# Kernel tuning notes

Hardware: AMD Instinct MI355X
Metric: run time of the kernel (lower is better)

Reference implementation:

```python
import jax, jax.numpy as jnp
import numpy as np

D_MODEL = 768
NUM_HEADS = 12
D_K = D_MODEL // NUM_HEADS
B, S = 2, 4096


def setup_inputs() -> dict:
    key = jax.random.key(0)
    ks = jax.random.split(key, 11)
    lim = 1.0 / np.sqrt(D_MODEL)  # torch Linear default init range
    def lin(k1, k2):
        W = jax.random.uniform(k1, (D_MODEL, D_MODEL), jnp.float32, -lim, lim)
        b = jax.random.uniform(k2, (D_MODEL,), jnp.float32, -lim, lim)
        return W, b
    Wq, bq = lin(ks[0], ks[1])
    Wk, bk = lin(ks[2], ks[3])
    Wv, bv = lin(ks[4], ks[5])
    Wo, bo = lin(ks[6], ks[7])
    Q = jax.random.normal(ks[8], (B, S, D_MODEL), jnp.float32)
    K = jax.random.normal(ks[9], (B, S, D_MODEL), jnp.float32)
    V = jax.random.normal(ks[10], (B, S, D_MODEL), jnp.float32)
    return {"Q": Q, "K": K, "V": V,
            "Wq": Wq, "bq": bq, "Wk": Wk, "bk": bk,
            "Wv": Wv, "bv": bv, "Wo": Wo, "bo": bo}


def reference(Q, K, V, Wq, bq, Wk, bk, Wv, bv, Wo, bo):
    def split_heads(x):
        b, s, _ = x.shape
        return x.reshape(b, s, NUM_HEADS, D_K).transpose(0, 2, 1, 3)  # [B,H,S,d_k]

    q = split_heads(Q @ Wq.T + bq)
    k = split_heads(K @ Wk.T + bk)
    v = split_heads(V @ Wv.T + bv)

    scale = 1.0 / np.sqrt(D_K).astype(np.float32)
    scores = jnp.einsum('bhqd,bhkd->bhqk', q, k) * scale  # [B,H,S,S]
    probs = jax.nn.softmax(scores, axis=-1)
    attn = jnp.einsum('bhqk,bhkd->bhqd', probs, v)  # [B,H,S,d_k]

    out = attn.transpose(0, 2, 1, 3).reshape(Q.shape[0], Q.shape[1], D_MODEL)
    return out @ Wo.T + bo
```

## Files before the change

### kernel.cpp

```cpp
#include <hip/hip_runtime.h>
#include <hip/hip_bf16.h>
#include <stdint.h>

#define DM 768
#define DK 64
#define NH 12
#define SQ 4096
#define BB 2

typedef __attribute__((ext_vector_type(8))) short bf16x8;
typedef __attribute__((ext_vector_type(4))) float f32x4;
typedef __attribute__((ext_vector_type(16))) float f32x16;
typedef __attribute__((ext_vector_type(4))) unsigned short u16x4;
typedef __attribute__((ext_vector_type(4))) unsigned int u32x4;
typedef unsigned short u16;
typedef unsigned int   u32;

__device__ __forceinline__ u16 f2bf(float f) {
    u32 u = __builtin_bit_cast(u32, f);
    u32 r = (u + 0x7fffu + ((u >> 16) & 1u)) >> 16;
    return (u16)r;
}
__device__ __forceinline__ u32 pack_trunc(float lo, float hi) {
    return __builtin_amdgcn_perm(__builtin_bit_cast(u32, hi),
                                 __builtin_bit_cast(u32, lo), 0x07060302u);
}
__device__ __forceinline__ void gl_lds16(const u16* g, u16* l) {
    __builtin_amdgcn_global_load_lds(
        (const __attribute__((address_space(1))) void*)g,
        (__attribute__((address_space(3))) void*)l, 16, 0, 0);
}

__global__ __launch_bounds__(256) void cvt_w(
    const float* __restrict__ W0, const float* __restrict__ W1,
    const float* __restrict__ W2, const float* __restrict__ W3,
    u16* __restrict__ d0, u16* __restrict__ d1,
    u16* __restrict__ d2, u16* __restrict__ d3)
{
    const float* s = blockIdx.y == 0 ? W0 : blockIdx.y == 1 ? W1
                   : blockIdx.y == 2 ? W2 : W3;
    u16* d        = blockIdx.y == 0 ? d0 : blockIdx.y == 1 ? d1
                   : blockIdx.y == 2 ? d2 : d3;
    size_t i = ((size_t)blockIdx.x * 256 + threadIdx.x) * 8;
    float4 a = *(const float4*)&s[i];
    float4 b = *(const float4*)&s[i + 4];
    u16x4 lo, hi;
    lo.x = f2bf(a.x); lo.y = f2bf(a.y); lo.z = f2bf(a.z); lo.w = f2bf(a.w);
    hi.x = f2bf(b.x); hi.y = f2bf(b.y); hi.z = f2bf(b.z); hi.w = f2bf(b.w);
    *(u16x4*)&d[i]     = lo;
    *(u16x4*)&d[i + 4] = hi;
}

#define BM 128
#define BN 128

__global__ __launch_bounds__(256) void gemm_qkv(
    const float* __restrict__ A0, const float* __restrict__ A1,
    const float* __restrict__ A2,
    const u16* __restrict__ W0, const u16* __restrict__ W1,
    const u16* __restrict__ W2,
    const float* __restrict__ b0, const float* __restrict__ b1,
    const float* __restrict__ b2,
    u16* __restrict__ qo, u16* __restrict__ ko, u16* __restrict__ vto,
    float qscale)
{
    __shared__ __align__(16) u16 Asm[2][BM * 32];
    __shared__ __align__(16) u16 Bsm[2][BM * 32];

    const int tid  = threadIdx.x;
    const int lane = tid & 63;
    const int w    = tid >> 6;
    const int wr   = w >> 1, wc = w & 1;
    const int l16  = lane & 15, lg = lane >> 4;

    const int ntiles = DM / BN;
    const int mt = blockIdx.x / ntiles;
    const int nt = blockIdx.x % ntiles;
    const int m0 = mt * BM, n0 = nt * BN;

    const int op = blockIdx.y;
    const float* A    = op == 0 ? A0 : op == 1 ? A1 : A2;
    const u16*  W     = op == 0 ? W0 : op == 1 ? W1 : W2;
    const float* bias = op == 0 ? b0 : op == 1 ? b1 : b2;
    const float oscale = op == 0 ? qscale : 1.0f;

    f32x4 acc[4][4];
    #pragma unroll
    for (int mi = 0; mi < 4; ++mi)
        #pragma unroll
        for (int ni = 0; ni < 4; ++ni)
            #pragma unroll
            for (int r = 0; r < 4; ++r) acc[mi][ni][r] = 0.f;

    #define GSTAGE(K0, B)                                                      \
        do {                                                                   \
            _Pragma("unroll")                                                  \
            for (int i_ = 0; i_ < 2; ++i_) {                                   \
                int c_   = (i_ * 4 + w) * 64 + lane;                           \
                int row_ = c_ >> 2;                                            \
                int col_ = ((c_ & 3) ^ (row_ & 3)) * 8;                        \
                gl_lds16(&W[(size_t)(n0 + row_) * DM + (K0) + col_],           \
                         &Bsm[B][(i_ * 4 + w) * 512]);                         \
            }                                                                  \
            _Pragma("unroll")                                                  \
            for (int i_ = 0; i_ < 2; ++i_) {                                   \
                int s_   = tid + i_ * 256;                                     \
                int row_ = s_ >> 2;                                            \
                int col_ = ((s_ & 3) ^ (row_ & 3)) * 8;                        \
                float4 x_ = *(const float4*)&A[(size_t)(m0 + row_) * DM + (K0) + col_];     \
                float4 y_ = *(const float4*)&A[(size_t)(m0 + row_) * DM + (K0) + col_ + 4]; \
                u16x4 lo_, hi_;                                                \
                lo_.x = f2bf(x_.x); lo_.y = f2bf(x_.y);                        \
                lo_.z = f2bf(x_.z); lo_.w = f2bf(x_.w);                        \
                hi_.x = f2bf(y_.x); hi_.y = f2bf(y_.y);                        \
                hi_.z = f2bf(y_.z); hi_.w = f2bf(y_.w);                        \
                *(u16x4*)&Asm[B][s_ * 8]     = lo_;                            \
                *(u16x4*)&Asm[B][s_ * 8 + 4] = hi_;                            \
            }                                                                  \
        } while (0)

    GSTAGE(0, 0);

    for (int kk = 0; kk < DM / 32; ++kk) {
        __syncthreads();
        if (kk + 1 < DM / 32) GSTAGE((kk + 1) * 32, (kk + 1) & 1);

        const u16* Ab = Asm[kk & 1];
        const u16* Bb = Bsm[kk & 1];
        bf16x8 af[4], bfr[4];
        #pragma unroll
        for (int mi = 0; mi < 4; ++mi) {
            int r = wr * 64 + mi * 16 + l16;
            af[mi] = *(const bf16x8*)((const char*)Ab + (size_t)r * 64
                                      + (((lg ^ r) & 3) << 4));
        }
        #pragma unroll
        for (int ni = 0; ni < 4; ++ni) {
            int r = wc * 64 + ni * 16 + l16;
            bfr[ni] = *(const bf16x8*)((const char*)Bb + (size_t)r * 64
                                       + (((lg ^ r) & 3) << 4));
        }

        #pragma unroll
        for (int mi = 0; mi < 4; ++mi)
            #pragma unroll
            for (int ni = 0; ni < 4; ++ni)
                acc[mi][ni] = __builtin_amdgcn_mfma_f32_16x16x32_bf16(
                    af[mi], bfr[ni], acc[mi][ni], 0, 0, 0);
    }
    #undef GSTAGE

    #pragma unroll
    for (int mi = 0; mi < 4; ++mi)
        #pragma unroll
        for (int ni = 0; ni < 4; ++ni) {
            int n = n0 + wc * 64 + ni * 16 + l16;
            float bv = bias[n];
            if (op == 2) {
                int hh = n >> 6, dd = n & 63;
                int mb = m0 + wr * 64 + mi * 16 + lg * 4;
                int bI = mb >> 12;
                int kv = mb & (SQ - 1);
                int kvs = (kv & ~12) | ((kv & 4) << 1) | ((kv & 8) >> 1);
                u16x4 pk;
                #pragma unroll
                for (int r = 0; r < 4; ++r)
                    pk[r] = f2bf(acc[mi][ni][r] + bv);
                *(u16x4*)&vto[(((size_t)bI * NH + hh) * DK + dd) * SQ + kvs] = pk;
            } else {
                u16* out = op ? ko : qo;
                #pragma unroll
                for (int r = 0; r < 4; ++r) {
                    int m = m0 + wr * 64 + mi * 16 + lg * 4 + r;
                    out[(size_t)m * DM + n] = f2bf((acc[mi][ni][r] + bv) * oscale);
                }
            }
        }
}

__global__ __launch_bounds__(256) void gemm_out(
    const u16* __restrict__ A, const u16* __restrict__ W,
    const float* __restrict__ bias, float* __restrict__ C)
{
    __shared__ __align__(16) u16 Asm[2][64 * 32];
    __shared__ __align__(16) u16 Bsm[2][128 * 32];

    const int tid  = threadIdx.x;
    const int lane = tid & 63;
    const int w    = tid >> 6;
    const int wr   = w >> 1, wc = w & 1;
    const int l16  = lane & 15, lg = lane >> 4;

    const int ntiles = DM / 128;
    const int mt = blockIdx.x / ntiles;
    const int nt = blockIdx.x % ntiles;
    const int m0 = mt * 64, n0 = nt * 128;

    f32x4 acc[2][4];
    #pragma unroll
    for (int mi = 0; mi < 2; ++mi)
        #pragma unroll
        for (int ni = 0; ni < 4; ++ni)
            #pragma unroll
            for (int r = 0; r < 4; ++r) acc[mi][ni][r] = 0.f;

    #define OSTAGE(K0, B)                                                      \
        do {                                                                   \
            _Pragma("unroll")                                                  \
            for (int i_ = 0; i_ < 2; ++i_) {                                   \
                int c_   = (i_ * 4 + w) * 64 + lane;                           \
                int row_ = c_ >> 2;                                            \
                int col_ = ((c_ & 3) ^ (row_ & 3)) * 8;                        \
                gl_lds16(&W[(size_t)(n0 + row_) * DM + (K0) + col_],           \
                         &Bsm[B][(i_ * 4 + w) * 512]);                         \
            }                                                                  \
            {                                                                  \
                int c_   = w * 64 + lane;                                      \
                int row_ = c_ >> 2;                                            \
                int col_ = ((c_ & 3) ^ (row_ & 3)) * 8;                        \
                gl_lds16(&A[(size_t)(m0 + row_) * DM + (K0) + col_],           \
                         &Asm[B][w * 512]);                                    \
            }                                                                  \
        } while (0)

    OSTAGE(0, 0);

    for (int kk = 0; kk < DM / 32; ++kk) {
        __syncthreads();
        if (kk + 1 < DM / 32) OSTAGE((kk + 1) * 32, (kk + 1) & 1);

        const u16* Ab = Asm[kk & 1];
        const u16* Bb = Bsm[kk & 1];
        bf16x8 af[2], bfr[4];
        #pragma unroll
        for (int mi = 0; mi < 2; ++mi) {
            int r = wr * 32 + mi * 16 + l16;
            af[mi] = *(const bf16x8*)((const char*)Ab + (size_t)r * 64
                                      + (((lg ^ r) & 3) << 4));
        }
        #pragma unroll
        for (int ni = 0; ni < 4; ++ni) {
            int r = wc * 64 + ni * 16 + l16;
            bfr[ni] = *(const bf16x8*)((const char*)Bb + (size_t)r * 64
                                       + (((lg ^ r) & 3) << 4));
        }

        #pragma unroll
        for (int mi = 0; mi < 2; ++mi)
            #pragma unroll
            for (int ni = 0; ni < 4; ++ni)
                acc[mi][ni] = __builtin_amdgcn_mfma_f32_16x16x32_bf16(
                    af[mi], bfr[ni], acc[mi][ni], 0, 0, 0);
    }
    #undef OSTAGE

    #pragma unroll
    for (int mi = 0; mi < 2; ++mi)
        #pragma unroll
        for (int ni = 0; ni < 4; ++ni) {
            int n = n0 + wc * 64 + ni * 16 + l16;
            float bv = bias[n];
            #pragma unroll
            for (int r = 0; r < 4; ++r) {
                int m = m0 + wr * 32 + mi * 16 + lg * 4 + r;
                C[(size_t)m * DM + n] = acc[mi][ni][r] + bv;
            }
        }
}

__global__ __launch_bounds__(512) void flash_attn_db(
    const u16* __restrict__ Qm, const u16* __restrict__ Km,
    const u16* __restrict__ VT, u16* __restrict__ Om)
{
    __shared__ __align__(16) char ldsbuf[65536];

    const int tid  = threadIdx.x;
    const int lane = tid & 63;
    const int w    = tid >> 6;
    const int qg   = w & 3;
    const int half = w >> 2;
    const int kvL  = lane & 31;
    const int hi   = lane >> 5;

    const int bid = blockIdx.x;
    const int grp = bid >> 3;
    const int bh  = (bid & 7) * 3 + (grp >> 5);
    const int qt  = grp & 31;
    const int b   = bh / NH, h = bh % NH;
    const size_t baseQ  = (size_t)b * SQ * DM + (size_t)h * DK;
    const size_t baseVT = (size_t)bh * DK * SQ;

    const int q = qt * 128 + qg * 32 + kvL;

    bf16x8 qf[4];
    #pragma unroll
    for (int j = 0; j < 4; ++j)
        qf[j] = *(const bf16x8*)&Qm[baseQ + (size_t)q * DM + j * 16 + hi * 8];

    int off[4];
    #pragma unroll
    for (int j = 0; j < 4; ++j)
        off[j] = kvL * 128 + (((2 * j + hi) ^ (kvL & 7)) << 4);

    int srow[2], schk[2];
    #pragma unroll
    for (int i = 0; i < 2; ++i) {
        int r = (qg * 2 + i) * 8 + (lane >> 3);
        srow[i] = r;
        schk[i] = (((lane & 7) ^ (r & 7)) << 3);
    }

    f32x16 accO[2];
    #pragma unroll
    for (int e = 0; e < 16; ++e) { accO[0][e] = 0.f; accO[1][e] = 0.f; }
    float lrun = 0.f;

    #define STAGE(T, B)                                                        \
        do {                                                                   \
            int kv0_ = (T) * 128 + half * 64;                                  \
            u16* KL_ = (u16*)(ldsbuf + (B) * 32768 + half * 16384);            \
            u16* VL_ = (u16*)(ldsbuf + (B) * 32768 + half * 16384 + 8192);     \
            _Pragma("unroll")                                                  \
            for (int i_ = 0; i_ < 2; ++i_) {                                   \
                gl_lds16(&Km[baseQ + (size_t)(kv0_ + srow[i_]) * DM + schk[i_]], \
                         KL_ + (qg * 2 + i_) * 512);                           \
                gl_lds16(&VT[baseVT + (size_t)srow[i_] * SQ + kv0_ + schk[i_]], \
                         VL_ + (qg * 2 + i_) * 512);                           \
            }                                                                  \
        } while (0)

    STAGE(0, 0);

    for (int t = 0; t < SQ / 128; ++t) {
        __syncthreads();
        if (t + 1 < SQ / 128) STAGE(t + 1, (t + 1) & 1);

        const char* KB = ldsbuf + (t & 1) * 32768 + half * 16384;
        const char* VB = KB + 8192;

        f32x16 s0, s1;
        #pragma unroll
        for (int e = 0; e < 16; ++e) { s0[e] = 0.f; s1[e] = 0.f; }
        __builtin_amdgcn_s_setprio(1);
        #pragma unroll
        for (int j = 0; j < 4; ++j) {
            bf16x8 kf0 = *(const bf16x8*)(KB + off[j]);
            bf16x8 kf1 = *(const bf16x8*)(KB + 4096 + off[j]);
            s0 = __builtin_amdgcn_mfma_f32_32x32x16_bf16(kf0, qf[j], s0, 0, 0, 0);
            s1 = __builtin_amdgcn_mfma_f32_32x32x16_bf16(kf1, qf[j], s1, 0, 0, 0);
        }
        __builtin_amdgcn_s_setprio(0);

        u32 pb[16];
        float rs0 = 0.f, rs1 = 0.f;
        #pragma unroll
        for (int wd = 0; wd < 8; ++wd) {
            float a0 = __builtin_amdgcn_exp2f(s0[2 * wd]);
            float a1 = __builtin_amdgcn_exp2f(s0[2 * wd + 1]);
            float b0 = __builtin_amdgcn_exp2f(s1[2 * wd]);
            float b1 = __builtin_amdgcn_exp2f(s1[2 * wd + 1]);
            rs0 += a0 + a1;
            rs1 += b0 + b1;
            pb[wd]     = pack_trunc(a0, a1);
            pb[8 + wd] = pack_trunc(b0, b1);
        }
        lrun += rs0 + rs1;

        __builtin_amdgcn_s_setprio(1);
        #pragma unroll
        for (int m = 0; m < 4; ++m) {
            int sb = 4 * m;
            u32x4 wds;
            wds[0] = pb[sb + 0];
            wds[1] = pb[sb + 1];
            wds[2] = pb[sb + 2];
            wds[3] = pb[sb + 3];
            bf16x8 Bp = __builtin_bit_cast(bf16x8, wds);
            bf16x8 v0 = *(const bf16x8*)(VB + off[m]);
            bf16x8 v1 = *(const bf16x8*)(VB + 4096 + off[m]);
            accO[0] = __builtin_amdgcn_mfma_f32_32x32x16_bf16(v0, Bp, accO[0], 0, 0, 0);
            accO[1] = __builtin_amdgcn_mfma_f32_32x32x16_bf16(v1, Bp, accO[1], 0, 0, 0);
        }
        __builtin_amdgcn_s_setprio(0);
    }
    #undef STAGE

    __syncthreads();

    lrun = lrun + __shfl_xor(lrun, 32);

    float* mo = (float*)ldsbuf;
    float* ml = (float*)(ldsbuf + 34816);
    const int rowi = (qg * 32 + kvL);

    if (half == 1) {
        float* row = mo + rowi * 68;
        #pragma unroll
        for (int c = 0; c < 2; ++c)
            #pragma unroll
            for (int e = 0; e < 16; ++e)
                row[(e >> 2) * 8 + (e & 3) + hi * 4 + c * 32] = accO[c][e];
        if (hi == 0) ml[rowi] = lrun;
    }
    __syncthreads();
    if (half == 0) {
        float* row = mo + rowi * 68;
        float inv = 1.f / (lrun + ml[rowi]);
        #pragma unroll
        for (int c = 0; c < 2; ++c)
            #pragma unroll
            for (int t4 = 0; t4 < 4; ++t4) {
                int d0 = t4 * 8 + hi * 4 + c * 32;
                u16x4 pk;
                #pragma unroll
                for (int u = 0; u < 4; ++u) {
                    float val = (accO[c][t4 * 4 + u] + row[d0 + u]) * inv;
                    pk[u] = f2bf(val);
                }
                *(u16x4*)&Om[baseQ + (size_t)q * DM + d0] = pk;
            }
    }
}

extern "C" void kernel_launch(void* const* d_in, const int* in_sizes, int n_in,
                              void* d_out, int out_size, void* d_ws, size_t ws_size,
                              hipStream_t stream)
{
    const float* Q  = (const float*)d_in[0];
    const float* K  = (const float*)d_in[1];
    const float* V  = (const float*)d_in[2];
    const float* Wq = (const float*)d_in[3];
    const float* bq = (const float*)d_in[4];
    const float* Wk = (const float*)d_in[5];
    const float* bk = (const float*)d_in[6];
    const float* Wv = (const float*)d_in[7];
    const float* bv = (const float*)d_in[8];
    const float* Wo = (const float*)d_in[9];
    const float* bo = (const float*)d_in[10];
    (void)in_sizes; (void)n_in; (void)out_size; (void)ws_size;

    const size_t E  = (size_t)BB * SQ * DM;
    const size_t WE = (size_t)DM * DM;
    u16* qws  = (u16*)d_ws;
    u16* kws  = qws + E;
    u16* vtws = kws + E;
    u16* aws  = vtws + E;
    u16* wqb  = aws + E;
    u16* wkb  = wqb + WE;
    u16* wvb  = wkb + WE;
    u16* wob  = wvb + WE;

    const float qscale = 0.125f * 1.4426950408889634f;

    hipLaunchKernelGGL(cvt_w, dim3(WE / 2048, 4), dim3(256), 0, stream,
                       Wq, Wk, Wv, Wo, wqb, wkb, wvb, wob);

    dim3 gq((BB * SQ / BM) * (DM / BN), 3);
    hipLaunchKernelGGL(gemm_qkv, gq, dim3(256), 0, stream,
                       Q, K, V, wqb, wkb, wvb, bq, bk, bv,
                       qws, kws, vtws, qscale);

    dim3 ga(768);
    hipLaunchKernelGGL(flash_attn_db, ga, dim3(512), 0, stream, qws, kws, vtws, aws);

    dim3 gg((BB * SQ / 64) * (DM / 128));
    hipLaunchKernelGGL(gemm_out, gg, dim3(256), 0, stream, aws, wob, bo, (float*)d_out);
}
```

Measured before the change: 220.6 us.

## Drop KV-split across wave halves in flash attention, use 256-thread blocks

The attention kernel no longer splits each 128-key tile between two groups of four waves. It now uses four waves per block that each process every 64-key tile, with a 32KB double-buffered LDS instead of 64KB. This removes the cross-half LDS reduction and its extra barriers at the end, and the smaller LDS footprint may let more blocks fit per CU. In exchange, each wave runs twice as many loop iterations, and there are twice as many per-tile barriers for the same amount of work.

```diff
diff --git a/kernel.cpp b/kernel.cpp
--- a/kernel.cpp
+++ b/kernel.cpp
@@ -268,17 +268,15 @@
         }
 }
 
-__global__ __launch_bounds__(512) void flash_attn_db(
+__global__ __launch_bounds__(256) void flash_attn_v11(
     const u16* __restrict__ Qm, const u16* __restrict__ Km,
     const u16* __restrict__ VT, u16* __restrict__ Om)
 {
-    __shared__ __align__(16) char ldsbuf[65536];
+    __shared__ __align__(16) char ldsbuf[32768];
 
     const int tid  = threadIdx.x;
     const int lane = tid & 63;
     const int w    = tid >> 6;
-    const int qg   = w & 3;
-    const int half = w >> 2;
     const int kvL  = lane & 31;
     const int hi   = lane >> 5;
 
@@ -290,7 +288,7 @@
     const size_t baseQ  = (size_t)b * SQ * DM + (size_t)h * DK;
     const size_t baseVT = (size_t)bh * DK * SQ;
 
-    const int q = qt * 128 + qg * 32 + kvL;
+    const int q = qt * 128 + w * 32 + kvL;
 
     bf16x8 qf[4];
     #pragma unroll
@@ -302,13 +300,8 @@
     for (int j = 0; j < 4; ++j)
         off[j] = kvL * 128 + (((2 * j + hi) ^ (kvL & 7)) << 4);
 
-    int srow[2], schk[2];
-    #pragma unroll
-    for (int i = 0; i < 2; ++i) {
-        int r = (qg * 2 + i) * 8 + (lane >> 3);
-        srow[i] = r;
-        schk[i] = (((lane & 7) ^ (r & 7)) << 3);
-    }
+    const int r0  = w * 16 + (lane >> 3);
+    const int chk = (((lane & 7) ^ (r0 & 7)) << 3);
 
     f32x16 accO[2];
     #pragma unroll
@@ -317,25 +310,26 @@
 
     #define STAGE(T, B)                                                        \
         do {                                                                   \
-            int kv0_ = (T) * 128 + half * 64;                                  \
-            u16* KL_ = (u16*)(ldsbuf + (B) * 32768 + half * 16384);            \
-            u16* VL_ = (u16*)(ldsbuf + (B) * 32768 + half * 16384 + 8192);     \
-            _Pragma("unroll")                                                  \
-            for (int i_ = 0; i_ < 2; ++i_) {                                   \
-                gl_lds16(&Km[baseQ + (size_t)(kv0_ + srow[i_]) * DM + schk[i_]], \
-                         KL_ + (qg * 2 + i_) * 512);                           \
-                gl_lds16(&VT[baseVT + (size_t)srow[i_] * SQ + kv0_ + schk[i_]], \
-                         VL_ + (qg * 2 + i_) * 512);                           \
-            }                                                                  \
+            int kv0_ = (T) * 64;                                               \
+            u16* KL_ = (u16*)(ldsbuf + (B) * 16384);                           \
+            u16* VL_ = (u16*)(ldsbuf + (B) * 16384 + 8192);   \
+            gl_lds16(&Km[baseQ + (size_t)(kv0_ + r0) * DM + chk],              \
+                     KL_ + (w * 2) * 512);                                     \
+            gl_lds16(&Km[baseQ + (size_t)(kv0_ + r0 + 8) * DM + chk],          \
+                     KL_ + (w * 2 + 1) * 512);                                 \
+            gl_lds16(&VT[baseVT + (size_t)r0 * SQ + kv0_ + chk],               \
+                     VL_ + (w * 2) * 512);                                     \
+            gl_lds16(&VT[baseVT + (size_t)(r0 + 8) * SQ + kv0_ + chk],         \
+                     VL_ + (w * 2 + 1) * 512);                                 \
         } while (0)
 
     STAGE(0, 0);
 
-    for (int t = 0; t < SQ / 128; ++t) {
+    for (int t = 0; t < SQ / 64; ++t) {
         __syncthreads();
-        if (t + 1 < SQ / 128) STAGE(t + 1, (t + 1) & 1);
-
-        const char* KB = ldsbuf + (t & 1) * 32768 + half * 16384;
+        if (t + 1 < SQ / 64) STAGE(t + 1, (t + 1) & 1);
+
+        const char* KB = ldsbuf + (t & 1) * 16384;
         const char* VB = KB + 8192;
 
         f32x16 s0, s1;
@@ -385,41 +379,20 @@
     }
     #undef STAGE
 
-    __syncthreads();
-
     lrun = lrun + __shfl_xor(lrun, 32);
-
-    float* mo = (float*)ldsbuf;
-    float* ml = (float*)(ldsbuf + 34816);
-    const int rowi = (qg * 32 + kvL);
-
-    if (half == 1) {
-        float* row = mo + rowi * 68;
-        #pragma unroll
-        for (int c = 0; c < 2; ++c)
-            #pragma unroll
-            for (int e = 0; e < 16; ++e)
-                row[(e >> 2) * 8 + (e & 3) + hi * 4 + c * 32] = accO[c][e];
-        if (hi == 0) ml[rowi] = lrun;
-    }
-    __syncthreads();
-    if (half == 0) {
-        float* row = mo + rowi * 68;
-        float inv = 1.f / (lrun + ml[rowi]);
-        #pragma unroll
-        for (int c = 0; c < 2; ++c)
-            #pragma unroll
-            for (int t4 = 0; t4 < 4; ++t4) {
-                int d0 = t4 * 8 + hi * 4 + c * 32;
-                u16x4 pk;
-                #pragma unroll
-                for (int u = 0; u < 4; ++u) {
-                    float val = (accO[c][t4 * 4 + u] + row[d0 + u]) * inv;
-                    pk[u] = f2bf(val);
-                }
-                *(u16x4*)&Om[baseQ + (size_t)q * DM + d0] = pk;
-            }
-    }
+    float inv = 1.f / lrun;
+
+    #pragma unroll
+    for (int c = 0; c < 2; ++c)
+        #pragma unroll
+        for (int t4 = 0; t4 < 4; ++t4) {
+            int d0 = t4 * 8 + hi * 4 + c * 32;
+            u16x4 pk;
+            #pragma unroll
+            for (int u = 0; u < 4; ++u)
+                pk[u] = f2bf(accO[c][t4 * 4 + u] * inv);
+            *(u16x4*)&Om[baseQ + (size_t)q * DM + d0] = pk;
+        }
 }
 
 extern "C" void kernel_launch(void* const* d_in, const int* in_sizes, int n_in,
@@ -461,7 +434,7 @@
                        qws, kws, vtws, qscale);
 
     dim3 ga(768);
-    hipLaunchKernelGGL(flash_attn_db, ga, dim3(512), 0, stream, qws, kws, vtws, aws);
+    hipLaunchKernelGGL(flash_attn_v11, ga, dim3(256), 0, stream, qws, kws, vtws, aws);
 
     dim3 gg((BB * SQ / 64) * (DM / 128));
     hipLaunchKernelGGL(gemm_out, gg, dim3(256), 0, stream, aws, wob, bo, (float*)d_out);
```

After: 244.0 us. 10.6% more time.
